# Optimization experiments

Measured on AMD Instinct MI355X. Metric: run time of the kernel, lower is better.

Reference implementation:

```python
import jax, jax.numpy as jnp
import numpy as np

N_QUBITS = 4
Q_LAYERS = 3
BATCH = 16384


def setup_inputs() -> dict:
    key = jax.random.key(0)
    ks = jax.random.split(key, 12)

    def n(k, shape, s=0.1):
        return (s * jax.random.normal(k, shape)).astype(jnp.float32)

    return {
        "x": jax.random.normal(ks[0], (BATCH, 1, 28, 28), jnp.float32),
        "conv1_w": n(ks[1], (6, 1, 5, 5)),
        "conv1_b": n(ks[2], (6,)),
        "conv2_w": n(ks[3], (16, 6, 5, 5)),
        "conv2_b": n(ks[4], (16,)),
        "fc1_w": n(ks[5], (120, 256)),
        "fc1_b": n(ks[6], (120,)),
        "fc2_w": n(ks[7], (N_QUBITS, 120)),
        "fc2_b": n(ks[8], (N_QUBITS,)),
        "q_weights": n(ks[9], (Q_LAYERS, 1, N_QUBITS, 3), 0.01),
        "clf_w": n(ks[10], (10, N_QUBITS)),
        "clf_b": n(ks[11], (10,)),
    }


def _apply_1q(state, U, w):
    # state: (B, 2,2,2,2); U: (2,2) shared or (B,2,2) per-sample
    s = jnp.moveaxis(state, 1 + w, -1)
    if U.ndim == 2:
        s = jnp.einsum('ij,...j->...i', U, s)
    else:
        s = jnp.einsum('bij,b...j->b...i', U, s)
    return jnp.moveaxis(s, -1, 1 + w)


def _cnot(state, c, t):
    s = jnp.moveaxis(state, (1 + c, 1 + t), (-2, -1))
    s = jnp.concatenate([s[..., 0:1, :], s[..., 1:2, ::-1]], axis=-2)
    return jnp.moveaxis(s, (-2, -1), (1 + c, 1 + t))


def _rot(phi, theta, omega):
    # PennyLane Rot = RZ(omega) @ RY(theta) @ RZ(phi)
    c = jnp.cos(theta / 2)
    s = jnp.sin(theta / 2)
    m00 = jnp.exp(-0.5j * (phi + omega)) * c
    m01 = -jnp.exp(0.5j * (phi - omega)) * s
    m10 = jnp.exp(0.5j * (omega - phi)) * s
    m11 = jnp.exp(0.5j * (phi + omega)) * c
    return jnp.stack([jnp.stack([m00, m01]), jnp.stack([m10, m11])])


def _rx(a):
    # a: (B,) -> (B,2,2) RX matrices
    c = jnp.cos(a / 2) + 0j
    z = -1j * jnp.sin(a / 2)
    return jnp.stack([jnp.stack([c, z], -1), jnp.stack([z, c], -1)], -2)


def _circuit(angles, qw):
    # Data-reuploading circuit: per block, StronglyEntanglingLayers(1 sublayer, r=1)
    # then AngleEmbedding (RX). Returns <Z_i> per qubit, shape (B, 4).
    Bn = angles.shape[0]
    state = jnp.zeros((Bn, 16), jnp.complex64).at[:, 0].set(1.0)
    state = state.reshape(Bn, 2, 2, 2, 2)
    n_layers = qw.shape[0]
    for l in range(n_layers):
        for w in range(N_QUBITS):
            state = _apply_1q(state, _rot(qw[l, 0, w, 0], qw[l, 0, w, 1], qw[l, 0, w, 2]), w)
        for w in range(N_QUBITS):
            state = _cnot(state, w, (w + 1) % N_QUBITS)
        for w in range(N_QUBITS):
            state = _apply_1q(state, _rx(angles[:, w]), w)
    probs = jnp.abs(state) ** 2
    z = []
    for w in range(N_QUBITS):
        p = jnp.moveaxis(probs, 1 + w, -1).reshape(Bn, -1, 2)
        z.append(p[..., 0].sum(-1) - p[..., 1].sum(-1))
    return jnp.stack(z, axis=1).astype(jnp.float32)


def _conv(x, w, b):
    y = jax.lax.conv_general_dilated(x, w, (1, 1), 'VALID',
                                     dimension_numbers=('NCHW', 'OIHW', 'NCHW'))
    return y + b[None, :, None, None]


def _pool(x):
    return jax.lax.reduce_window(x, -jnp.inf, jax.lax.max,
                                 (1, 1, 2, 2), (1, 1, 2, 2), 'VALID')


def reference(x, conv1_w, conv1_b, conv2_w, conv2_b, fc1_w, fc1_b,
              fc2_w, fc2_b, q_weights, clf_w, clf_b):
    h = _pool(jax.nn.relu(_conv(x, conv1_w, conv1_b)))       # (B,6,12,12)
    h = _pool(jax.nn.relu(_conv(h, conv2_w, conv2_b)))       # (B,16,4,4)
    h = h.reshape(h.shape[0], -1)                            # (B,256)
    h = jax.nn.relu(h @ fc1_w.T + fc1_b)                     # (B,120)
    feat = h @ fc2_w.T + fc2_b                               # (B,4)
    angles = jnp.pi * jax.nn.sigmoid(feat)
    q_out = _circuit(angles, q_weights)                      # (B,4)
    logits = q_out @ clf_w.T + clf_b                         # (B,10)
    return logits
```

## Files before the change

### kernel.cpp

```cpp
#include <hip/hip_runtime.h>
#include <math.h>

#define BATCH_N 16384

typedef _Float16 half8 __attribute__((ext_vector_type(8)));
typedef __fp16 h2 __attribute__((ext_vector_type(2)));
typedef float f32x4 __attribute__((ext_vector_type(4)));

#define C1P_F  0
#define BS1_F  120
#define BS2_F  128
#define ROTM_F 144
#define RXCS_F 240
#define CWB_F  368
#define W2B_F  420
#define PW_F   2276
#define LDS_FLOATS 10020

#define WV_STRIDE_H 3872
#define XH_SAMP_H   784
#define H1_OFF_H    1568
#define H1_SAMP_H   1152
#define H2A_ROW_H   264
#define HS_OFF_H    4224
#define HS_ROW_H    136

static __device__ __forceinline__ h2 u2h(unsigned u) {
    union { unsigned u; h2 h; } c; c.u = u; return c.h;
}

struct Row5 { h2 a0, a1, a2, s0, s1; };
static __device__ __forceinline__ Row5 ldrow(const unsigned* xw) {
    const unsigned u0 = xw[0], u1 = xw[1], u2 = xw[2];
    Row5 r;
    r.a0 = u2h(u0); r.a1 = u2h(u1); r.a2 = u2h(u2);
    r.s0 = u2h((u0 >> 16) | (u1 << 16));
    r.s1 = u2h((u1 >> 16) | (u2 << 16));
    return r;
}

__global__ __launch_bounds__(256, 4) void fused_model(
    const float* __restrict__ xg,
    const float* __restrict__ c1w, const float* __restrict__ c1b,
    const float* __restrict__ c2w, const float* __restrict__ c2b,
    const float* __restrict__ f1w, const float* __restrict__ f1b,
    const float* __restrict__ f2w, const float* __restrict__ f2b,
    const float* __restrict__ qw,  const float* __restrict__ cw,
    const float* __restrict__ cbias, float* __restrict__ out) {
    __shared__ float L[LDS_FLOATS];
    const int tid = threadIdx.x;
    const int b0 = blockIdx.x * 16;
    const int lane = tid & 63, wvi = tid >> 6;
    const int ml = lane & 15, q = lane >> 4;

    _Float16* W2BH = (_Float16*)(L + W2B_F);
    _Float16* PWH  = (_Float16*)(L + PW_F);
    _Float16* XHH  = PWH + wvi * WV_STRIDE_H;
    _Float16* H1CH = XHH + H1_OFF_H;
    _Float16* H2AH = PWH;
    _Float16* HSH  = PWH + HS_OFF_H;

    if (tid < 120) {
        const int oc = tid / 20, r = tid - oc * 20, ky = r >> 2, j = r & 3;
        const float* wb = c1w + oc * 25 + ky * 5;
        float lo, hi;
        if (j == 0)      { lo = wb[0]; hi = wb[1]; }
        else if (j == 1) { lo = wb[2]; hi = wb[3]; }
        else if (j == 2) { lo = wb[4]; hi = 0.f;   }
        else             { lo = 0.f;   hi = wb[4]; }
        ((h2*)&L[C1P_F])[tid] = __builtin_amdgcn_cvt_pkrtz(lo, hi);
    }
    if (tid < 6)  L[BS1_F + tid] = c1b[tid];
    if (tid < 16) L[BS2_F + tid] = c2b[tid];
    if (tid < 40) L[CWB_F + tid] = cw[tid];
    if (tid < 10) L[CWB_F + 40 + tid] = cbias[tid];
    if (tid < 12) {
        const float phi = qw[tid * 3 + 0];
        const float th  = qw[tid * 3 + 1];
        const float om  = qw[tid * 3 + 2];
        const float ct = cosf(0.5f * th), st = sinf(0.5f * th);
        const float ap = 0.5f * (phi + om), bm = 0.5f * (phi - om);
        const float ca = cosf(ap), sa = sinf(ap);
        const float cbm = cosf(bm), sbm = sinf(bm);
        float* R = &L[ROTM_F + tid * 8];
        R[0] =  ct * ca;  R[1] = -ct * sa;
        R[2] = -st * cbm; R[3] = -st * sbm;
        R[4] =  st * cbm; R[5] = -st * sbm;
        R[6] =  ct * ca;  R[7] =  ct * sa;
    }
    {
        int oc = (tid >= 232) ? 1 : 0;
        int r = tid - oc * 232;
#pragma unroll 1
        for (int i = tid; i < 3712; i += 256) {
            float v = 0.f;
            if (r < 200) {
                const int pix = r >> 3, ic = r & 7;
                if (ic < 6) v = c2w[oc * 150 + ic * 25 + pix];
            }
            W2BH[oc * 232 + r] = (_Float16)v;
            r += 24; oc += 1;
            if (r >= 232) { r -= 232; oc += 1; }
        }
    }
    __syncthreads();

    unsigned h2r[2][2][4];

#pragma unroll 2
    for (int p = 0; p < 2; ++p) {
        const int sbase = b0 + 4 * wvi + 2 * p;

        for (int k = lane; k < 392; k += 64) {
            const int s = (k >= 196) ? 1 : 0;
            const int kk = k - 196 * s;
            const int row = kk / 7, q4 = kk - row * 7;
            const float4 v = *(const float4*)(xg + (size_t)(sbase + s) * 784 + row * 28 + q4 * 4);
            union { h2 h[2]; uint2 u; } W;
            W.h[0] = __builtin_amdgcn_cvt_pkrtz(v.x, v.y);
            W.h[1] = __builtin_amdgcn_cvt_pkrtz(v.z, v.w);
            *(uint2*)(XHH + s * XH_SAMP_H + row * 28 + q4 * 4) = W.u;
        }
        __builtin_amdgcn_wave_barrier();

        for (int t = lane; t < 288; t += 64) {
            const int s = t >= 144 ? 1 : 0;
            const int r = t - s * 144;
            const int py = r / 12, px = r - (r / 12) * 12;
            const unsigned* xw = (const unsigned*)(XHH + s * XH_SAMP_H) + 2 * py * 14 + px;

            float acc[6][4];
#pragma unroll
            for (int oc = 0; oc < 6; oc++) {
                const float bv = L[BS1_F + oc];
                acc[oc][0] = bv; acc[oc][1] = bv; acc[oc][2] = bv; acc[oc][3] = bv;
            }

            Row5 R0 = ldrow(xw);
#pragma unroll
            for (int ky = 0; ky < 5; ky++) {
                const Row5 R1 = ldrow(xw + (ky + 1) * 14);
#pragma unroll
                for (int oc = 0; oc < 6; oc++) {
                    union { uint4 v; h2 h[4]; } W;
                    W.v = ((const uint4*)&L[C1P_F])[oc * 5 + ky];
                    acc[oc][0] = __builtin_amdgcn_fdot2(R0.a0, W.h[0], acc[oc][0], false);
                    acc[oc][0] = __builtin_amdgcn_fdot2(R0.a1, W.h[1], acc[oc][0], false);
                    acc[oc][0] = __builtin_amdgcn_fdot2(R0.a2, W.h[2], acc[oc][0], false);
                    acc[oc][1] = __builtin_amdgcn_fdot2(R0.s0, W.h[0], acc[oc][1], false);
                    acc[oc][1] = __builtin_amdgcn_fdot2(R0.s1, W.h[1], acc[oc][1], false);
                    acc[oc][1] = __builtin_amdgcn_fdot2(R0.a2, W.h[3], acc[oc][1], false);
                    acc[oc][2] = __builtin_amdgcn_fdot2(R1.a0, W.h[0], acc[oc][2], false);
                    acc[oc][2] = __builtin_amdgcn_fdot2(R1.a1, W.h[1], acc[oc][2], false);
                    acc[oc][2] = __builtin_amdgcn_fdot2(R1.a2, W.h[2], acc[oc][2], false);
                    acc[oc][3] = __builtin_amdgcn_fdot2(R1.s0, W.h[0], acc[oc][3], false);
                    acc[oc][3] = __builtin_amdgcn_fdot2(R1.s1, W.h[1], acc[oc][3], false);
                    acc[oc][3] = __builtin_amdgcn_fdot2(R1.a2, W.h[3], acc[oc][3], false);
                }
                R0 = R1;
            }

            union { _Float16 h[8]; uint4 u; } O;
#pragma unroll
            for (int oc = 0; oc < 6; oc++) {
                const float m = fmaxf(fmaxf(acc[oc][0], acc[oc][1]), fmaxf(acc[oc][2], acc[oc][3]));
                O.h[oc] = (_Float16)fmaxf(m, 0.f);
            }
            O.h[6] = (_Float16)0.f; O.h[7] = (_Float16)0.f;
            *(uint4*)(H1CH + s * H1_SAMP_H + (py * 12 + px) * 8) = O.u;
        }
        __builtin_amdgcn_wave_barrier();

        {
            f32x4 c2a[2][4];
#pragma unroll
            for (int a = 0; a < 2; a++)
#pragma unroll
                for (int b = 0; b < 4; b++) c2a[a][b] = (f32x4){0.f, 0.f, 0.f, 0.f};

#pragma unroll
            for (int ks = 0; ks < 7; ks++) {
                const half8 bfrag = *(const half8*)(W2BH + ml * 232 + ks * 32 + q * 8);
                int tp = ks * 4 + q; if (tp > 24) tp = 24;
                const int poff = (tp / 5) * 12 + (tp % 5);
#pragma unroll
                for (int si = 0; si < 2; si++) {
                    const _Float16* hp = H1CH + si * H1_SAMP_H;
#pragma unroll
                    for (int t = 0; t < 4; t++) {
                        const int cp = t * 16 + ml;
                        const int unit = (cp >> 3) * 12 + (cp & 7) + poff;
                        const half8 afrag = *(const half8*)(hp + unit * 8);
                        c2a[si][t] = __builtin_amdgcn_mfma_f32_16x16x32_f16(afrag, bfrag, c2a[si][t], 0, 0, 0);
                    }
                }
            }

            const float bv = L[BS2_F + ml];
#pragma unroll
            for (int si = 0; si < 2; si++) {
#pragma unroll
                for (int t = 0; t < 4; t++) {
                    const float c0 = c2a[si][t][0] + bv, c1 = c2a[si][t][1] + bv;
                    const float c2 = c2a[si][t][2] + bv, c3 = c2a[si][t][3] + bv;
                    float px0 = fmaxf(c0, c1), px1 = fmaxf(c2, c3);
                    px0 = fmaxf(px0, __shfl_xor(px0, 32));
                    px1 = fmaxf(px1, __shfl_xor(px1, 32));
                    union { _Float16 h[2]; unsigned u; } P2;
                    P2.h[0] = (_Float16)fmaxf(px0, 0.f);
                    P2.h[1] = (_Float16)fmaxf(px1, 0.f);
                    h2r[p][si][t] = P2.u;
                }
            }
        }
        __builtin_amdgcn_wave_barrier();
    }
    __syncthreads();

    if (lane < 32) {
#pragma unroll
        for (int p = 0; p < 2; p++)
#pragma unroll
            for (int si = 0; si < 2; si++)
#pragma unroll
                for (int t = 0; t < 4; t++) {
                    const int srow = 4 * wvi + 2 * p + si;
                    *(unsigned*)(H2AH + srow * H2A_ROW_H + ml * 16 + t * 4 + q * 2) = h2r[p][si][t];
                }
    }
    __syncthreads();

    {
        f32x4 fcC[2];
        fcC[0] = (f32x4){0.f, 0.f, 0.f, 0.f};
        fcC[1] = (f32x4){0.f, 0.f, 0.f, 0.f};
        const _Float16* h2p = H2AH + ml * H2A_ROW_H;
#pragma unroll
        for (int ks = 0; ks < 8; ks++) {
            const half8 afrag = *(const half8*)(h2p + ks * 32 + q * 8);
#pragma unroll
            for (int ti = 0; ti < 2; ti++) {
                const int n = (wvi + 4 * ti) * 16 + ml;
                half8 bfrag;
                if (n < 120) {
                    const float* wp = f1w + (size_t)n * 256 + ks * 32 + q * 8;
                    const float4 u = *(const float4*)wp;
                    const float4 v = *(const float4*)(wp + 4);
                    union { h2 p[4]; half8 h8; } B;
                    B.p[0] = __builtin_amdgcn_cvt_pkrtz(u.x, u.y);
                    B.p[1] = __builtin_amdgcn_cvt_pkrtz(u.z, u.w);
                    B.p[2] = __builtin_amdgcn_cvt_pkrtz(v.x, v.y);
                    B.p[3] = __builtin_amdgcn_cvt_pkrtz(v.z, v.w);
                    bfrag = B.h8;
                } else {
#pragma unroll
                    for (int j = 0; j < 8; j++) bfrag[j] = (_Float16)0.f;
                }
                fcC[ti] = __builtin_amdgcn_mfma_f32_16x16x32_f16(afrag, bfrag, fcC[ti], 0, 0, 0);
            }
        }
#pragma unroll
        for (int ti = 0; ti < 2; ti++) {
            const int n = (wvi + 4 * ti) * 16 + ml;
            if (n < 120) {
                const float bb = f1b[n];
#pragma unroll
                for (int rg = 0; rg < 4; rg++) {
                    const int s = q * 4 + rg;
                    HSH[s * HS_ROW_H + n] = (_Float16)fmaxf(fcC[ti][rg] + bb, 0.f);
                }
            }
        }
    }
    __syncthreads();

    {
        const int s = tid >> 4, m = (tid >> 2) & 3, part = tid & 3;
        float f = (part == 0) ? f2b[m] : 0.f;
#pragma unroll
        for (int i = 0; i < 4; ++i) {
            const int bblk = part + 4 * i;
            if (bblk < 15) {
                const half8 hv = *(const half8*)(HSH + s * HS_ROW_H + bblk * 8);
                const float* wp = f2w + m * 120 + bblk * 8;
                const float4 w0 = *(const float4*)wp;
                const float4 w1 = *(const float4*)(wp + 4);
                f = fmaf(w0.x, (float)hv[0], f); f = fmaf(w0.y, (float)hv[1], f);
                f = fmaf(w0.z, (float)hv[2], f); f = fmaf(w0.w, (float)hv[3], f);
                f = fmaf(w1.x, (float)hv[4], f); f = fmaf(w1.y, (float)hv[5], f);
                f = fmaf(w1.z, (float)hv[6], f); f = fmaf(w1.w, (float)hv[7], f);
            }
        }
        f += __shfl_xor(f, 1);
        f += __shfl_xor(f, 2);
        if (part == 0) {
            const float ang = 3.14159265358979323846f / (1.f + expf(-f));
            L[RXCS_F + s * 4 + m]      = cosf(0.5f * ang);
            L[RXCS_F + 64 + s * 4 + m] = sinf(0.5f * ang);
        }
    }
    __syncthreads();

    {
        const int s = tid >> 4, a = tid & 15;
        float ar = (a == 0) ? 1.f : 0.f, ai = 0.f;

#pragma unroll
        for (int l = 0; l < 3; l++) {
#pragma unroll
            for (int w = 0; w < 4; w++) {
                const float* R = &L[ROTM_F + (l * 4 + w) * 8];
                const int mask = 8 >> w;
                const float pr = __shfl_xor(ar, mask);
                const float pi = __shfl_xor(ai, mask);
                const bool bit = (a & mask) != 0;
                const float lr = bit ? pr : ar, li = bit ? pi : ai;
                const float hr = bit ? ar : pr, hi = bit ? ai : pi;
                const float Ar = bit ? R[4] : R[0], Ai = bit ? R[5] : R[1];
                const float Br = bit ? R[6] : R[2], Bi = bit ? R[7] : R[3];
                ar = Ar * lr - Ai * li + Br * hr - Bi * hi;
                ai = Ar * li + Ai * lr + Br * hi + Bi * hr;
            }
#pragma unroll
            for (int w = 0; w < 4; w++) {
                const int mc = 8 >> w, mt = 8 >> ((w + 1) & 3);
                const float pr = __shfl_xor(ar, mt);
                const float pi = __shfl_xor(ai, mt);
                const bool ctrl = (a & mc) != 0;
                ar = ctrl ? pr : ar;
                ai = ctrl ? pi : ai;
            }
#pragma unroll
            for (int w = 0; w < 4; w++) {
                const int mask = 8 >> w;
                const float c  = L[RXCS_F + s * 4 + w];
                const float s2 = L[RXCS_F + 64 + s * 4 + w];
                const float pr = __shfl_xor(ar, mask);
                const float pi = __shfl_xor(ai, mask);
                const float nr = fmaf(c, ar, s2 * pi);
                const float ni = fmaf(c, ai, -s2 * pr);
                ar = nr; ai = ni;
            }
        }

        float v = ar * ar + ai * ai;
#pragma unroll
        for (int d = 1; d < 16; d <<= 1) {
            const float pv = __shfl_xor(v, d);
            v = (a & d) ? (pv - v) : (v + pv);
        }

        if (a < 10) {
            const int base = (tid & 63) & ~15;
            float lg = L[CWB_F + 40 + a];
#pragma unroll
            for (int w = 0; w < 4; w++) {
                const float zw = __shfl(v, base | (8 >> w));
                lg = fmaf(L[CWB_F + a * 4 + w], zw, lg);
            }
            out[(size_t)(b0 + s) * 10 + a] = lg;
        }
    }
}

extern "C" void kernel_launch(void* const* d_in, const int* in_sizes, int n_in,
                              void* d_out, int out_size, void* d_ws, size_t ws_size,
                              hipStream_t stream) {
    const float* x   = (const float*)d_in[0];
    const float* c1w = (const float*)d_in[1];
    const float* c1b = (const float*)d_in[2];
    const float* c2w = (const float*)d_in[3];
    const float* c2b = (const float*)d_in[4];
    const float* f1w = (const float*)d_in[5];
    const float* f1b = (const float*)d_in[6];
    const float* f2w = (const float*)d_in[7];
    const float* f2b = (const float*)d_in[8];
    const float* qw  = (const float*)d_in[9];
    const float* cw  = (const float*)d_in[10];
    const float* cb  = (const float*)d_in[11];
    float* out = (float*)d_out;

    fused_model<<<BATCH_N / 16, 256, 0, stream>>>(x, c1w, c1b, c2w, c2b,
                                                  f1w, f1b, f2w, f2b,
                                                  qw, cw, cb, out);
}
```

Measured before the change: 162.5 us.

## Use 512-thread blocks with two samples per wave and direct global conv1 input reads

Doubles the block size to 8 waves, so each wave handles 2 samples instead of 4 and the fc1 MFMA tiles are split one per wave. Conv1 now reads input rows straight from global memory and converts them to fp16 in registers, removing the per-wave LDS staging of the image. Pool2 results go directly to LDS instead of being held in registers until an extra barrier. The aim is more parallelism, less LDS traffic and a lower LDS footprint, at the cost of redundant global loads of overlapping input rows and idle threads in the tail stages.

```diff
diff --git a/kernel.cpp b/kernel.cpp
--- a/kernel.cpp
+++ b/kernel.cpp
@@ -14,32 +14,26 @@
 #define RXCS_F 240
 #define CWB_F  368
 #define W2B_F  420
-#define PW_F   2276
-#define LDS_FLOATS 10020
-
-#define WV_STRIDE_H 3872
-#define XH_SAMP_H   784
-#define H1_OFF_H    1568
-#define H1_SAMP_H   1152
-#define H2A_ROW_H   264
-#define HS_OFF_H    4224
-#define HS_ROW_H    136
-
-static __device__ __forceinline__ h2 u2h(unsigned u) {
-    union { unsigned u; h2 h; } c; c.u = u; return c.h;
-}
+#define H2A_F  2276
+#define PW_F   4388
+#define LDS_FLOATS 8996
+
+#define H1_WV_H   1152
+#define H2A_ROW_H 264
+#define HS_ROW_H  136
 
 struct Row5 { h2 a0, a1, a2, s0, s1; };
-static __device__ __forceinline__ Row5 ldrow(const unsigned* xw) {
-    const unsigned u0 = xw[0], u1 = xw[1], u2 = xw[2];
+static __device__ __forceinline__ Row5 packrow(float4 a, float2 c) {
     Row5 r;
-    r.a0 = u2h(u0); r.a1 = u2h(u1); r.a2 = u2h(u2);
-    r.s0 = u2h((u0 >> 16) | (u1 << 16));
-    r.s1 = u2h((u1 >> 16) | (u2 << 16));
+    r.a0 = __builtin_amdgcn_cvt_pkrtz(a.x, a.y);
+    r.a1 = __builtin_amdgcn_cvt_pkrtz(a.z, a.w);
+    r.a2 = __builtin_amdgcn_cvt_pkrtz(c.x, c.y);
+    r.s0 = __builtin_amdgcn_cvt_pkrtz(a.y, a.z);
+    r.s1 = __builtin_amdgcn_cvt_pkrtz(a.w, c.x);
     return r;
 }
 
-__global__ __launch_bounds__(256, 4) void fused_model(
+__global__ __launch_bounds__(512, 8) void fused_model(
     const float* __restrict__ xg,
     const float* __restrict__ c1w, const float* __restrict__ c1b,
     const float* __restrict__ c2w, const float* __restrict__ c2b,
@@ -54,11 +48,9 @@
     const int ml = lane & 15, q = lane >> 4;
 
     _Float16* W2BH = (_Float16*)(L + W2B_F);
-    _Float16* PWH  = (_Float16*)(L + PW_F);
-    _Float16* XHH  = PWH + wvi * WV_STRIDE_H;
-    _Float16* H1CH = XHH + H1_OFF_H;
-    _Float16* H2AH = PWH;
-    _Float16* HSH  = PWH + HS_OFF_H;
+    _Float16* H2AH = (_Float16*)(L + H2A_F);
+    _Float16* H1CH = (_Float16*)(L + PW_F) + wvi * H1_WV_H;
+    _Float16* HSH  = (_Float16*)(L + PW_F);
 
     if (tid < 120) {
         const int oc = tid / 20, r = tid - oc * 20, ky = r >> 2, j = r & 3;
@@ -88,46 +80,25 @@
         R[4] =  st * cbm; R[5] = -st * sbm;
         R[6] =  ct * ca;  R[7] =  ct * sa;
     }
-    {
-        int oc = (tid >= 232) ? 1 : 0;
-        int r = tid - oc * 232;
 #pragma unroll 1
-        for (int i = tid; i < 3712; i += 256) {
-            float v = 0.f;
-            if (r < 200) {
-                const int pix = r >> 3, ic = r & 7;
-                if (ic < 6) v = c2w[oc * 150 + ic * 25 + pix];
-            }
-            W2BH[oc * 232 + r] = (_Float16)v;
-            r += 24; oc += 1;
-            if (r >= 232) { r -= 232; oc += 1; }
-        }
+    for (int i = tid; i < 3712; i += 512) {
+        const int oc = i / 232, r = i - oc * 232;
+        float v = 0.f;
+        if (r < 200) {
+            const int pix = r >> 3, ic = r & 7;
+            if (ic < 6) v = c2w[oc * 150 + ic * 25 + pix];
+        }
+        W2BH[oc * 232 + r] = (_Float16)v;
     }
     __syncthreads();
 
-    unsigned h2r[2][2][4];
-
-#pragma unroll 2
-    for (int p = 0; p < 2; ++p) {
-        const int sbase = b0 + 4 * wvi + 2 * p;
-
-        for (int k = lane; k < 392; k += 64) {
-            const int s = (k >= 196) ? 1 : 0;
-            const int kk = k - 196 * s;
-            const int row = kk / 7, q4 = kk - row * 7;
-            const float4 v = *(const float4*)(xg + (size_t)(sbase + s) * 784 + row * 28 + q4 * 4);
-            union { h2 h[2]; uint2 u; } W;
-            W.h[0] = __builtin_amdgcn_cvt_pkrtz(v.x, v.y);
-            W.h[1] = __builtin_amdgcn_cvt_pkrtz(v.z, v.w);
-            *(uint2*)(XHH + s * XH_SAMP_H + row * 28 + q4 * 4) = W.u;
-        }
-        __builtin_amdgcn_wave_barrier();
-
-        for (int t = lane; t < 288; t += 64) {
-            const int s = t >= 144 ? 1 : 0;
-            const int r = t - s * 144;
-            const int py = r / 12, px = r - (r / 12) * 12;
-            const unsigned* xw = (const unsigned*)(XHH + s * XH_SAMP_H) + 2 * py * 14 + px;
+#pragma unroll 1
+    for (int s = 0; s < 2; ++s) {
+        const int smp = b0 + 2 * wvi + s;
+
+        for (int t = lane; t < 144; t += 64) {
+            const int py = t / 12, px = t - (t / 12) * 12;
+            const float* xp = xg + (size_t)smp * 784 + py * 56 + px * 2;
 
             float acc[6][4];
 #pragma unroll
@@ -136,28 +107,34 @@
                 acc[oc][0] = bv; acc[oc][1] = bv; acc[oc][2] = bv; acc[oc][3] = bv;
             }
 
-            Row5 R0 = ldrow(xw);
+            Row5 P0 = packrow(*(const float4*)xp, *(const float2*)(xp + 4));
+            Row5 P1 = packrow(*(const float4*)(xp + 28), *(const float2*)(xp + 32));
 #pragma unroll
             for (int ky = 0; ky < 5; ky++) {
-                const Row5 R1 = ldrow(xw + (ky + 1) * 14);
+                float4 A; float2 C;
+                if (ky < 4) {
+                    A = *(const float4*)(xp + (ky + 2) * 28);
+                    C = *(const float2*)(xp + (ky + 2) * 28 + 4);
+                }
 #pragma unroll
                 for (int oc = 0; oc < 6; oc++) {
                     union { uint4 v; h2 h[4]; } W;
                     W.v = ((const uint4*)&L[C1P_F])[oc * 5 + ky];
-                    acc[oc][0] = __builtin_amdgcn_fdot2(R0.a0, W.h[0], acc[oc][0], false);
-                    acc[oc][0] = __builtin_amdgcn_fdot2(R0.a1, W.h[1], acc[oc][0], false);
-                    acc[oc][0] = __builtin_amdgcn_fdot2(R0.a2, W.h[2], acc[oc][0], false);
-                    acc[oc][1] = __builtin_amdgcn_fdot2(R0.s0, W.h[0], acc[oc][1], false);
-                    acc[oc][1] = __builtin_amdgcn_fdot2(R0.s1, W.h[1], acc[oc][1], false);
-                    acc[oc][1] = __builtin_amdgcn_fdot2(R0.a2, W.h[3], acc[oc][1], false);
-                    acc[oc][2] = __builtin_amdgcn_fdot2(R1.a0, W.h[0], acc[oc][2], false);
-                    acc[oc][2] = __builtin_amdgcn_fdot2(R1.a1, W.h[1], acc[oc][2], false);
-                    acc[oc][2] = __builtin_amdgcn_fdot2(R1.a2, W.h[2], acc[oc][2], false);
-                    acc[oc][3] = __builtin_amdgcn_fdot2(R1.s0, W.h[0], acc[oc][3], false);
-                    acc[oc][3] = __builtin_amdgcn_fdot2(R1.s1, W.h[1], acc[oc][3], false);
-                    acc[oc][3] = __builtin_amdgcn_fdot2(R1.a2, W.h[3], acc[oc][3], false);
+                    acc[oc][0] = __builtin_amdgcn_fdot2(P0.a0, W.h[0], acc[oc][0], false);
+                    acc[oc][0] = __builtin_amdgcn_fdot2(P0.a1, W.h[1], acc[oc][0], false);
+                    acc[oc][0] = __builtin_amdgcn_fdot2(P0.a2, W.h[2], acc[oc][0], false);
+                    acc[oc][1] = __builtin_amdgcn_fdot2(P0.s0, W.h[0], acc[oc][1], false);
+                    acc[oc][1] = __builtin_amdgcn_fdot2(P0.s1, W.h[1], acc[oc][1], false);
+                    acc[oc][1] = __builtin_amdgcn_fdot2(P0.a2, W.h[3], acc[oc][1], false);
+                    acc[oc][2] = __builtin_amdgcn_fdot2(P1.a0, W.h[0], acc[oc][2], false);
+                    acc[oc][2] = __builtin_amdgcn_fdot2(P1.a1, W.h[1], acc[oc][2], false);
+                    acc[oc][2] = __builtin_amdgcn_fdot2(P1.a2, W.h[2], acc[oc][2], false);
+                    acc[oc][3] = __builtin_amdgcn_fdot2(P1.s0, W.h[0], acc[oc][3], false);
+                    acc[oc][3] = __builtin_amdgcn_fdot2(P1.s1, W.h[1], acc[oc][3], false);
+                    acc[oc][3] = __builtin_amdgcn_fdot2(P1.a2, W.h[3], acc[oc][3], false);
                 }
-                R0 = R1;
+                P0 = P1;
+                if (ky < 4) P1 = packrow(A, C);
             }
 
             union { _Float16 h[8]; uint4 u; } O;
@@ -167,16 +144,14 @@
                 O.h[oc] = (_Float16)fmaxf(m, 0.f);
             }
             O.h[6] = (_Float16)0.f; O.h[7] = (_Float16)0.f;
-            *(uint4*)(H1CH + s * H1_SAMP_H + (py * 12 + px) * 8) = O.u;
+            *(uint4*)(H1CH + (py * 12 + px) * 8) = O.u;
         }
         __builtin_amdgcn_wave_barrier();
 
         {
-            f32x4 c2a[2][4];
-#pragma unroll
-            for (int a = 0; a < 2; a++)
-#pragma unroll
-                for (int b = 0; b < 4; b++) c2a[a][b] = (f32x4){0.f, 0.f, 0.f, 0.f};
+            f32x4 c2a[4];
+#pragma unroll
+            for (int b = 0; b < 4; b++) c2a[b] = (f32x4){0.f, 0.f, 0.f, 0.f};
 
 #pragma unroll
             for (int ks = 0; ks < 7; ks++) {
@@ -184,32 +159,27 @@
                 int tp = ks * 4 + q; if (tp > 24) tp = 24;
                 const int poff = (tp / 5) * 12 + (tp % 5);
 #pragma unroll
-                for (int si = 0; si < 2; si++) {
-                    const _Float16* hp = H1CH + si * H1_SAMP_H;
-#pragma unroll
-                    for (int t = 0; t < 4; t++) {
-                        const int cp = t * 16 + ml;
-                        const int unit = (cp >> 3) * 12 + (cp & 7) + poff;
-                        const half8 afrag = *(const half8*)(hp + unit * 8);
-                        c2a[si][t] = __builtin_amdgcn_mfma_f32_16x16x32_f16(afrag, bfrag, c2a[si][t], 0, 0, 0);
-                    }
+                for (int t = 0; t < 4; t++) {
+                    const int cp = t * 16 + ml;
+                    const int unit = (cp >> 3) * 12 + (cp & 7) + poff;
+                    const half8 afrag = *(const half8*)(H1CH + unit * 8);
+                    c2a[t] = __builtin_amdgcn_mfma_f32_16x16x32_f16(afrag, bfrag, c2a[t], 0, 0, 0);
                 }
             }
 
             const float bv = L[BS2_F + ml];
 #pragma unroll
-            for (int si = 0; si < 2; si++) {
-#pragma unroll
-                for (int t = 0; t < 4; t++) {
-                    const float c0 = c2a[si][t][0] + bv, c1 = c2a[si][t][1] + bv;
-                    const float c2 = c2a[si][t][2] + bv, c3 = c2a[si][t][3] + bv;
-                    float px0 = fmaxf(c0, c1), px1 = fmaxf(c2, c3);
-                    px0 = fmaxf(px0, __shfl_xor(px0, 32));
-                    px1 = fmaxf(px1, __shfl_xor(px1, 32));
+            for (int t = 0; t < 4; t++) {
+                const float c0 = c2a[t][0] + bv, c1 = c2a[t][1] + bv;
+                const float c2 = c2a[t][2] + bv, c3 = c2a[t][3] + bv;
+                float px0 = fmaxf(c0, c1), px1 = fmaxf(c2, c3);
+                px0 = fmaxf(px0, __shfl_xor(px0, 32));
+                px1 = fmaxf(px1, __shfl_xor(px1, 32));
+                if (lane < 32) {
                     union { _Float16 h[2]; unsigned u; } P2;
                     P2.h[0] = (_Float16)fmaxf(px0, 0.f);
                     P2.h[1] = (_Float16)fmaxf(px1, 0.f);
-                    h2r[p][si][t] = P2.u;
+                    *(unsigned*)(H2AH + (2 * wvi + s) * H2A_ROW_H + ml * 16 + t * 4 + (q & 1) * 2) = P2.u;
                 }
             }
         }
@@ -217,64 +187,40 @@
     }
     __syncthreads();
 
-    if (lane < 32) {
-#pragma unroll
-        for (int p = 0; p < 2; p++)
-#pragma unroll
-            for (int si = 0; si < 2; si++)
-#pragma unroll
-                for (int t = 0; t < 4; t++) {
-                    const int srow = 4 * wvi + 2 * p + si;
-                    *(unsigned*)(H2AH + srow * H2A_ROW_H + ml * 16 + t * 4 + q * 2) = h2r[p][si][t];
-                }
-    }
-    __syncthreads();
-
     {
-        f32x4 fcC[2];
-        fcC[0] = (f32x4){0.f, 0.f, 0.f, 0.f};
-        fcC[1] = (f32x4){0.f, 0.f, 0.f, 0.f};
+        f32x4 fcC = (f32x4){0.f, 0.f, 0.f, 0.f};
+        const int n = wvi * 16 + ml;
         const _Float16* h2p = H2AH + ml * H2A_ROW_H;
 #pragma unroll
         for (int ks = 0; ks < 8; ks++) {
             const half8 afrag = *(const half8*)(h2p + ks * 32 + q * 8);
-#pragma unroll
-            for (int ti = 0; ti < 2; ti++) {
-                const int n = (wvi + 4 * ti) * 16 + ml;
-                half8 bfrag;
-                if (n < 120) {
-                    const float* wp = f1w + (size_t)n * 256 + ks * 32 + q * 8;
-                    const float4 u = *(const float4*)wp;
-                    const float4 v = *(const float4*)(wp + 4);
-                    union { h2 p[4]; half8 h8; } B;
-                    B.p[0] = __builtin_amdgcn_cvt_pkrtz(u.x, u.y);
-                    B.p[1] = __builtin_amdgcn_cvt_pkrtz(u.z, u.w);
-                    B.p[2] = __builtin_amdgcn_cvt_pkrtz(v.x, v.y);
-                    B.p[3] = __builtin_amdgcn_cvt_pkrtz(v.z, v.w);
-                    bfrag = B.h8;
-                } else {
-#pragma unroll
-                    for (int j = 0; j < 8; j++) bfrag[j] = (_Float16)0.f;
-                }
-                fcC[ti] = __builtin_amdgcn_mfma_f32_16x16x32_f16(afrag, bfrag, fcC[ti], 0, 0, 0);
-            }
-        }
-#pragma unroll
-        for (int ti = 0; ti < 2; ti++) {
-            const int n = (wvi + 4 * ti) * 16 + ml;
+            half8 bfrag;
             if (n < 120) {
-                const float bb = f1b[n];
-#pragma unroll
-                for (int rg = 0; rg < 4; rg++) {
-                    const int s = q * 4 + rg;
-                    HSH[s * HS_ROW_H + n] = (_Float16)fmaxf(fcC[ti][rg] + bb, 0.f);
-                }
+                const float* wp = f1w + (size_t)n * 256 + ks * 32 + q * 8;
+                const float4 u = *(const float4*)wp;
+                const float4 v = *(const float4*)(wp + 4);
+                bfrag[0] = (_Float16)u.x; bfrag[1] = (_Float16)u.y;
+                bfrag[2] = (_Float16)u.z; bfrag[3] = (_Float16)u.w;
+                bfrag[4] = (_Float16)v.x; bfrag[5] = (_Float16)v.y;
+                bfrag[6] = (_Float16)v.z; bfrag[7] = (_Float16)v.w;
+            } else {
+#pragma unroll
+                for (int j = 0; j < 8; j++) bfrag[j] = (_Float16)0.f;
+            }
+            fcC = __builtin_amdgcn_mfma_f32_16x16x32_f16(afrag, bfrag, fcC, 0, 0, 0);
+        }
+        if (n < 120) {
+            const float bb = f1b[n];
+#pragma unroll
+            for (int rg = 0; rg < 4; rg++) {
+                const int sr = q * 4 + rg;
+                HSH[sr * HS_ROW_H + n] = (_Float16)fmaxf(fcC[rg] + bb, 0.f);
             }
         }
     }
     __syncthreads();
 
-    {
+    if (tid < 256) {
         const int s = tid >> 4, m = (tid >> 2) & 3, part = tid & 3;
         float f = (part == 0) ? f2b[m] : 0.f;
 #pragma unroll
@@ -301,7 +247,7 @@
     }
     __syncthreads();
 
-    {
+    if (tid < 256) {
         const int s = tid >> 4, a = tid & 15;
         float ar = (a == 0) ? 1.f : 0.f, ai = 0.f;
 
@@ -380,7 +326,7 @@
     const float* cb  = (const float*)d_in[11];
     float* out = (float*)d_out;
 
-    fused_model<<<BATCH_N / 16, 256, 0, stream>>>(x, c1w, c1b, c2w, c2b,
+    fused_model<<<BATCH_N / 16, 512, 0, stream>>>(x, c1w, c1b, c2w, c2b,
                                                   f1w, f1b, f2w, f2b,
                                                   qw, cw, cb, out);
 }
```

New measurement: 496.9 us. 206% more time.
